# Kernel tuning notes

Measured on AMD Instinct MI355X. Metric: run time of the kernel, lower is better.

## Reference

```python
import jax, jax.numpy as jnp
import numpy as np

B, L, D, H, NL, EXP = 8, 1024, 512, 8, 6, 4
DH = D // H
DF = D * EXP
EPS = 1e-3  # keras LayerNormalization default epsilon
NEG = -1e9  # keras Softmax mask adder for float32


def _ln(x, g, b):
    m = jnp.mean(x, axis=-1, keepdims=True)
    v = jnp.mean(jnp.square(x - m), axis=-1, keepdims=True)
    return (x - m) * jax.lax.rsqrt(v + EPS) * g + b


def _pos_emb(L, D):
    pos = jnp.arange(L, dtype=jnp.float32)[:, None]          # [L,1]
    i = jnp.arange(D // 2, dtype=jnp.float32)[None, :]        # [1,D/2]
    inv = jnp.power(10000.0, -2.0 * i / D)
    # original concatenates sin block then cos block along feature axis
    return jnp.concatenate([jnp.sin(pos * inv), jnp.cos(pos * inv)], axis=-1)  # [L,D]


def setup_inputs() -> dict:
    key = jax.random.key(0)
    ks = jax.random.split(key, 16)
    glorot = lambda k, shape: jax.random.uniform(
        k, shape, jnp.float32, -1.0, 1.0) * jnp.sqrt(6.0 / (shape[-2] + shape[-1]))
    return {
        "x": jax.random.normal(ks[0], (B, L, D), jnp.float32),
        "lengths": jax.random.randint(ks[1], (B,), L // 2, L + 1).astype(jnp.int32),
        "Wq": glorot(ks[2], (NL, D, D)),
        "Wk": glorot(ks[3], (NL, D, D)),
        "Wv": glorot(ks[4], (NL, D, D)),
        "Wo": glorot(ks[5], (NL, D, D)),
        "ln1_g": jnp.ones((NL, D), jnp.float32),
        "ln1_b": jnp.zeros((NL, D), jnp.float32),
        "ln2_g": jnp.ones((NL, D), jnp.float32),
        "ln2_b": jnp.zeros((NL, D), jnp.float32),
        "w1": glorot(ks[6], (NL, D, DF)),
        "b1": jnp.zeros((NL, DF), jnp.float32),
        "w2": glorot(ks[7], (NL, DF, D)),
        "b2": jnp.zeros((NL, D), jnp.float32),
    }


def _forward(x, mask_bias, Wq, Wk, Wv, Wo, ln1_g, ln1_b, ln2_g, ln2_b, w1, b1, w2, b2):
    x = x + _pos_emb(L, D)[None, :, :]
    scale = 1.0 / jnp.sqrt(jnp.float32(DH))

    def layer(x, p):
        wq, wk, wv, wo, g1, be1, g2, be2, fw1, fb1, fw2, fb2 = p
        h = _ln(x, g1, be1)
        split = lambda t: t.reshape(B, L, H, DH).transpose(0, 2, 1, 3)  # [B,H,L,DH]
        q, k, v = split(h @ wq), split(h @ wk), split(h @ wv)
        scores = jnp.einsum("bhqd,bhkd->bhqk", q, k) * scale + mask_bias
        attn = jax.nn.softmax(scores, axis=-1)
        o = jnp.einsum("bhqk,bhkd->bhqd", attn, v)
        o = o.transpose(0, 2, 1, 3).reshape(B, L, D) @ wo
        x = x + o  # dropout is identity at inference
        h2 = _ln(x, g2, be2)
        ffn = jax.nn.relu(h2 @ fw1 + fb1) @ fw2 + fb2
        return x + ffn, None

    x, _ = jax.lax.scan(layer, x, (Wq, Wk, Wv, Wo, ln1_g, ln1_b, ln2_g, ln2_b, w1, b1, w2, b2))
    return x


def reference(x, lengths, Wq, Wk, Wv, Wo, ln1_g, ln1_b, ln2_g, ln2_b, w1, b1, w2, b2):
    mask = (jnp.arange(L)[None, :] < lengths[:, None]).astype(jnp.float32)  # [B,L]
    mask_bias = (1.0 - mask)[:, None, None, :] * NEG                        # [B,1,1,L]
    return _forward(x, mask_bias, Wq, Wk, Wv, Wo, ln1_g, ln1_b, ln2_g, ln2_b, w1, b1, w2, b2)
```

## Files before the change

kernel.cpp:

```cpp
#include <hip/hip_runtime.h>
#include <cstdint>
#include <cstddef>

#define Bz 8
#define Lz 1024
#define Dz 512
#define Hz 8
#define NLz 6
#define DFz 2048
#define Mz (Bz*Lz)

typedef short bf16x8 __attribute__((ext_vector_type(8)));
typedef float f32x4  __attribute__((ext_vector_type(4)));
typedef short s16x4  __attribute__((ext_vector_type(4)));

__device__ __forceinline__ short f2bf(float f) {
    unsigned u = __builtin_bit_cast(unsigned, f);
    u = (u + 0x7fff + ((u >> 16) & 1)) >> 16;
    return (short)u;
}

__device__ __forceinline__ float exp2_fast(float x) {
#if __has_builtin(__builtin_amdgcn_exp2f)
    return __builtin_amdgcn_exp2f(x);
#else
    return exp2f(x);
#endif
}

#define GLD16(gp, lp) __builtin_amdgcn_global_load_lds( \
    (const __attribute__((address_space(1))) void*)(gp), \
    (__attribute__((address_space(3))) void*)(lp), 16, 0, 0)

__global__ __launch_bounds__(256) void posadd_kernel(const float* __restrict__ x,
                                                     float* __restrict__ y) {
    int idx = blockIdx.x * 256 + threadIdx.x;
    int d   = idx & (Dz - 1);
    int pos = (idx >> 9) & (Lz - 1);
    int i2  = (d < Dz/2) ? d : d - Dz/2;
    float inv = __expf(-0.03597789207f * (float)i2);
    float a = (float)pos * inv;
    float pe = (d < Dz/2) ? sinf(a) : cosf(a);
    y[idx] = x[idx] + pe;
}

__global__ __launch_bounds__(256) void ln_kernel(const float* __restrict__ x,
                                                 const float* __restrict__ g,
                                                 const float* __restrict__ b,
                                                 short* __restrict__ out) {
    int w = threadIdx.x >> 6, l = threadIdx.x & 63;
    int row = blockIdx.x * 4 + w;
    const float* xr = x + (size_t)row * Dz;
    f32x4 a0 = *(const f32x4*)(xr + l * 4);
    f32x4 a1 = *(const f32x4*)(xr + 256 + l * 4);
    float s = (a0[0] + a0[1]) + (a0[2] + a0[3]) + (a1[0] + a1[1]) + (a1[2] + a1[3]);
    #pragma unroll
    for (int off = 32; off; off >>= 1) s += __shfl_xor(s, off, 64);
    float m = s * (1.0f / Dz);
    f32x4 d0, d1;
    float s2 = 0.0f;
    #pragma unroll
    for (int j = 0; j < 4; j++) { d0[j] = a0[j] - m; s2 += d0[j] * d0[j]; }
    #pragma unroll
    for (int j = 0; j < 4; j++) { d1[j] = a1[j] - m; s2 += d1[j] * d1[j]; }
    #pragma unroll
    for (int off = 32; off; off >>= 1) s2 += __shfl_xor(s2, off, 64);
    float rs = rsqrtf(s2 * (1.0f / Dz) + 1e-3f);
    f32x4 g0 = *(const f32x4*)(g + l * 4);
    f32x4 g1 = *(const f32x4*)(g + 256 + l * 4);
    f32x4 b0 = *(const f32x4*)(b + l * 4);
    f32x4 b1 = *(const f32x4*)(b + 256 + l * 4);
    s16x4 o0, o1;
    #pragma unroll
    for (int j = 0; j < 4; j++) o0[j] = f2bf(d0[j] * rs * g0[j] + b0[j]);
    #pragma unroll
    for (int j = 0; j < 4; j++) o1[j] = f2bf(d1[j] * rs * g1[j] + b1[j]);
    *(s16x4*)(out + (size_t)row * Dz + l * 4)       = o0;
    *(s16x4*)(out + (size_t)row * Dz + 256 + l * 4) = o1;
}

__global__ __launch_bounds__(256) void transpose_bf16_kernel(const float* __restrict__ src,
                                                             short* __restrict__ dst,
                                                             int K, int N,
                                                             long srcLS, long dstLS, int rowOff) {
    __shared__ float tile[32][33];
    int tx = threadIdx.x & 31, ty = threadIdx.x >> 5;
    int bx = blockIdx.x, by = blockIdx.y, z = blockIdx.z;
    const float* s = src + (size_t)z * srcLS;
    short* d = dst + (size_t)z * dstLS;
    #pragma unroll
    for (int i = 0; i < 4; i++)
        tile[ty + i * 8][tx] = s[(size_t)(by * 32 + ty + i * 8) * N + bx * 32 + tx];
    __syncthreads();
    #pragma unroll
    for (int i = 0; i < 4; i++)
        d[(size_t)(rowOff + bx * 32 + ty + i * 8) * K + by * 32 + tx] = f2bf(tile[tx][ty + i * 8]);
}

__global__ __launch_bounds__(256) void vtrans_kernel(const short* __restrict__ qkv,
                                                     short* __restrict__ vbt) {
    int lt = blockIdx.x, bh = blockIdx.y;
    int b = bh >> 3, h = bh & 7;
    __shared__ short tile[64][72];
    int t = threadIdx.x;
    int l = t >> 2, c4 = t & 3;
    #pragma unroll
    for (int p = 0; p < 2; p++) {
        int dd = (c4 + p * 4) * 8;
        *(uint4*)&tile[l][dd] =
            *(const uint4*)(qkv + ((size_t)(b * Lz + lt * 64 + l)) * 1536 + 1024 + h * 64 + dd);
    }
    __syncthreads();
    int d = t >> 2;
    #pragma unroll
    for (int p = 0; p < 2; p++) {
        int lc = (c4 + p * 4) * 8;
        union { uint4 u; short s[8]; } o;
        #pragma unroll
        for (int j = 0; j < 8; j++) o.s[j] = tile[lc + j][d];
        *(uint4*)(vbt + ((size_t)(bh * 64 + d)) * Lz + lt * 64 + lc) = o.u;
    }
}

template<int MODE, int TN>
__global__ __launch_bounds__(256, 2)
void gemm_bt(const short* __restrict__ A,
             const short* __restrict__ Bt,
             short* __restrict__ outb,
             float* __restrict__ outf,
             float* __restrict__ outf2,
             const float* __restrict__ bias,
             int M, int N, int K) {
    constexpr int NI = TN / 32;
    __shared__ __attribute__((aligned(16))) short As[128 * 64];
    __shared__ __attribute__((aligned(16))) short Bs[TN * 64];
    int t = threadIdx.x;
    int m0 = blockIdx.x * 128, n0 = blockIdx.y * TN;
    int w = t >> 6, l = t & 63;
    int wm = (w >> 1) * 64, wn = (w & 1) * (TN / 2);
    int lr = l & 15, lq = l >> 4;
    f32x4 acc[4][NI] = {};
    int sr = t >> 3;
    int sc = ((t & 7) ^ (sr & 7)) * 8;
    for (int kk = 0; kk < K; kk += 64) {
        #pragma unroll
        for (int i = 0; i < 4; i++)
            GLD16(A + (size_t)(m0 + sr + i * 32) * K + kk + sc, As + i * 2048 + t * 8);
        #pragma unroll
        for (int i = 0; i < TN / 32; i++)
            GLD16(Bt + (size_t)(n0 + sr + i * 32) * K + kk + sc, Bs + i * 2048 + t * 8);
        __syncthreads();
        bf16x8 af[4][2], bfr[NI][2];
        #pragma unroll
        for (int i = 0; i < 4; i++) {
            int row = wm + i * 16 + lr;
            const short* rp = As + row * 64;
            af[i][0] = *(const bf16x8*)(rp + ((lq ^ (row & 7)) * 8));
            af[i][1] = *(const bf16x8*)(rp + (((4 + lq) ^ (row & 7)) * 8));
        }
        #pragma unroll
        for (int i = 0; i < NI; i++) {
            int row = wn + i * 16 + lr;
            const short* rp = Bs + row * 64;
            bfr[i][0] = *(const bf16x8*)(rp + ((lq ^ (row & 7)) * 8));
            bfr[i][1] = *(const bf16x8*)(rp + (((4 + lq) ^ (row & 7)) * 8));
        }
        #pragma unroll
        for (int mi = 0; mi < 4; mi++)
            #pragma unroll
            for (int ni = 0; ni < NI; ni++) {
                acc[mi][ni] = __builtin_amdgcn_mfma_f32_16x16x32_bf16(af[mi][0], bfr[ni][0], acc[mi][ni], 0, 0, 0);
                acc[mi][ni] = __builtin_amdgcn_mfma_f32_16x16x32_bf16(af[mi][1], bfr[ni][1], acc[mi][ni], 0, 0, 0);
            }
        __syncthreads();
    }
    #pragma unroll
    for (int mi = 0; mi < 4; mi++)
        #pragma unroll
        for (int ni = 0; ni < NI; ni++) {
            int col = n0 + wn + ni * 16 + lr;
            float bv = (MODE == 2 || MODE == 3 || MODE == 4) ? bias[col] : 0.0f;
            #pragma unroll
            for (int r = 0; r < 4; r++) {
                int row = m0 + wm + mi * 16 + lq * 4 + r;
                size_t idx = (size_t)row * N + col;
                float v = acc[mi][ni][r];
                if (MODE == 0)      outb[idx] = f2bf(v);
                else if (MODE == 1) outf[idx] += v;
                else if (MODE == 2) outb[idx] = f2bf(fmaxf(v + bv, 0.0f));
                else if (MODE == 3) outf[idx] += v + bv;
                else                outf2[idx] = outf[idx] + v + bv;
            }
        }
}

__device__ __forceinline__ void attn_frag(f32x4* sacc, const float* biask,
                                          float* mr, float* lsum, f32x4* oacc,
                                          short* Pw, const short* Vs,
                                          int lr, int lq, bf16x8 onesf) {
    const float SC2 = 0.18033688f;
    float p[8][4];
    #pragma unroll
    for (int r = 0; r < 4; r++) {
        float mx = -1e30f;
        #pragma unroll
        for (int kt = 0; kt < 8; kt++) {
            p[kt][r] = sacc[kt][r] * SC2 + biask[kt];
            mx = fmaxf(mx, p[kt][r]);
        }
        mx = fmaxf(mx, __shfl_xor(mx, 1, 64));
        mx = fmaxf(mx, __shfl_xor(mx, 2, 64));
        mx = fmaxf(mx, __shfl_xor(mx, 4, 64));
        mx = fmaxf(mx, __shfl_xor(mx, 8, 64));
        float mn = fmaxf(mr[r], mx);
        float alpha = exp2_fast(mr[r] - mn);
        mr[r] = mn;
        #pragma unroll
        for (int kt = 0; kt < 8; kt++)
            p[kt][r] = exp2_fast(p[kt][r] - mn);
        lsum[r] *= alpha;
        #pragma unroll
        for (int ni = 0; ni < 4; ni++) oacc[ni][r] *= alpha;
    }
    #pragma unroll
    for (int kt = 0; kt < 8; kt++)
        #pragma unroll
        for (int r = 0; r < 4; r++)
            Pw[(lq * 4 + r) * 136 + kt * 16 + lr] = f2bf(p[kt][r]);
    f32x4 sums = {};
    #pragma unroll
    for (int c = 0; c < 4; c++) {
        bf16x8 pf = *(const bf16x8*)(Pw + lr * 136 + c * 32 + lq * 8);
        sums = __builtin_amdgcn_mfma_f32_16x16x32_bf16(pf, onesf, sums, 0, 0, 0);
        #pragma unroll
        for (int ni = 0; ni < 4; ni++) {
            bf16x8 vf = *(const bf16x8*)(Vs + (ni * 16 + lr) * 136 + c * 32 + lq * 8);
            oacc[ni] = __builtin_amdgcn_mfma_f32_16x16x32_bf16(pf, vf, oacc[ni], 0, 0, 0);
        }
    }
    #pragma unroll
    for (int r = 0; r < 4; r++) lsum[r] += sums[r];
}

__global__ __launch_bounds__(256, 2) void attn_kernel(const short* __restrict__ qkv,
                                                      const short* __restrict__ vbt,
                                                      const int* __restrict__ lengths,
                                                      short* __restrict__ o) {
    __shared__ __attribute__((aligned(16))) short Ks[128 * 72];
    __shared__ __attribute__((aligned(16))) short Vs[64 * 136];
    __shared__ __attribute__((aligned(16))) short Ps[4][16 * 136];
    int qt = blockIdx.y;
    int bh = blockIdx.x;
    int b = bh >> 3, h = bh & 7;
    int len = lengths[b];
    int t = threadIdx.x, w = t >> 6, l = t & 63;
    int lr = l & 15, lq = l >> 4;

    const short* q0 = qkv + (size_t)(b * Lz + qt * 128 + w * 32 + lr) * 1536 + h * 64 + lq * 8;
    bf16x8 qf0a = *(const bf16x8*)(q0);
    bf16x8 qf0b = *(const bf16x8*)(q0 + 32);
    bf16x8 qf1a = *(const bf16x8*)(q0 + 16 * 1536);
    bf16x8 qf1b = *(const bf16x8*)(q0 + 16 * 1536 + 32);

    int kkey = t >> 3, kd8 = (t & 7) * 8;
    int vd = t >> 4, vk8 = (t & 15) * 8;
    const short* kbaseg = qkv + (size_t)(b * Lz) * 1536 + 512 + h * 64;
    const short* vbaseg = vbt + (size_t)(bh * 64) * Lz;

    float mr0[4] = {-1e30f, -1e30f, -1e30f, -1e30f}, ls0[4] = {0.f, 0.f, 0.f, 0.f};
    float mr1[4] = {-1e30f, -1e30f, -1e30f, -1e30f}, ls1[4] = {0.f, 0.f, 0.f, 0.f};
    f32x4 oacc0[4] = {}, oacc1[4] = {};
    bf16x8 onesf = {0x3F80, 0x3F80, 0x3F80, 0x3F80, 0x3F80, 0x3F80, 0x3F80, 0x3F80};

    uint4 kreg[4], vreg[4];
    #pragma unroll
    for (int i = 0; i < 4; i++)
        kreg[i] = *(const uint4*)(kbaseg + (size_t)(i * 32 + kkey) * 1536 + kd8);

    short* Pw = &Ps[w][0];
    int ntiles = (len + 127) >> 7;
    for (int tix = 0; tix < ntiles; tix++) {
        int k0 = tix << 7;
        __syncthreads();
        #pragma unroll
        for (int i = 0; i < 4; i++)
            *(uint4*)(Ks + (i * 32 + kkey) * 72 + kd8) = kreg[i];
        __syncthreads();
        #pragma unroll
        for (int i = 0; i < 4; i++)
            vreg[i] = *(const uint4*)(vbaseg + (size_t)(i * 16 + vd) * Lz + k0 + vk8);
        f32x4 sacc0[8] = {}, sacc1[8] = {};
        #pragma unroll
        for (int kt = 0; kt < 8; kt++) {
            bf16x8 kf0 = *(const bf16x8*)(Ks + (kt * 16 + lr) * 72 + lq * 8);
            bf16x8 kf1 = *(const bf16x8*)(Ks + (kt * 16 + lr) * 72 + 32 + lq * 8);
            sacc0[kt] = __builtin_amdgcn_mfma_f32_16x16x32_bf16(qf0a, kf0, sacc0[kt], 0, 0, 0);
            sacc0[kt] = __builtin_amdgcn_mfma_f32_16x16x32_bf16(qf0b, kf1, sacc0[kt], 0, 0, 0);
            sacc1[kt] = __builtin_amdgcn_mfma_f32_16x16x32_bf16(qf1a, kf0, sacc1[kt], 0, 0, 0);
            sacc1[kt] = __builtin_amdgcn_mfma_f32_16x16x32_bf16(qf1b, kf1, sacc1[kt], 0, 0, 0);
        }
        if (tix + 1 < ntiles) {
            #pragma unroll
            for (int i = 0; i < 4; i++)
                kreg[i] = *(const uint4*)(kbaseg + (size_t)(k0 + 128 + i * 32 + kkey) * 1536 + kd8);
        }
        #pragma unroll
        for (int i = 0; i < 4; i++)
            *(uint4*)(Vs + (i * 16 + vd) * 136 + vk8) = vreg[i];
        float biask[8];
        #pragma unroll
        for (int kt = 0; kt < 8; kt++)
            biask[kt] = ((k0 + kt * 16 + lr) < len) ? 0.0f : -1e30f;
        __syncthreads();
        attn_frag(sacc0, biask, mr0, ls0, oacc0, Pw, Vs, lr, lq, onesf);
        attn_frag(sacc1, biask, mr1, ls1, oacc1, Pw, Vs, lr, lq, onesf);
    }
    #pragma unroll
    for (int ni = 0; ni < 4; ni++)
        #pragma unroll
        for (int r = 0; r < 4; r++) {
            int q = qt * 128 + w * 32 + lq * 4 + r;
            size_t base = (size_t)(b * Lz + q) * Dz + h * 64 + ni * 16 + lr;
            o[base]             = f2bf(oacc0[ni][r] / ls0[r]);
            o[base + 16 * Dz]   = f2bf(oacc1[ni][r] / ls1[r]);
        }
}

extern "C" void kernel_launch(void* const* d_in, const int* in_sizes, int n_in,
                              void* d_out, int out_size, void* d_ws, size_t ws_size,
                              hipStream_t stream) {
    const float* x_in    = (const float*)d_in[0];
    const int*   lengths = (const int*)d_in[1];
    const float* Wq   = (const float*)d_in[2];
    const float* Wk   = (const float*)d_in[3];
    const float* Wv   = (const float*)d_in[4];
    const float* Wo   = (const float*)d_in[5];
    const float* ln1g = (const float*)d_in[6];
    const float* ln1b = (const float*)d_in[7];
    const float* ln2g = (const float*)d_in[8];
    const float* ln2b = (const float*)d_in[9];
    const float* w1   = (const float*)d_in[10];
    const float* b1   = (const float*)d_in[11];
    const float* w2   = (const float*)d_in[12];
    const float* b2   = (const float*)d_in[13];

    size_t off = 0;
    auto alloc = [&](size_t bytes) {
        void* p = (char*)d_ws + off;
        off += (bytes + 255) & ~(size_t)255;
        return p;
    };
    float* x_work = (float*)alloc((size_t)Mz * Dz * 4);
    short* hbuf   = (short*)alloc((size_t)Mz * Dz * 2);
    short* qkvb   = (short*)alloc((size_t)Mz * 1536 * 2);
    short* f1b    = (short*)alloc((size_t)Mz * DFz * 2);
    short* vbt    = (short*)alloc((size_t)Bz * Hz * 64 * Lz * 2);
    short* wqkvT  = (short*)alloc((size_t)NLz * 1536 * Dz * 2);
    short* woT    = (short*)alloc((size_t)NLz * Dz * Dz * 2);
    short* w1T    = (short*)alloc((size_t)NLz * DFz * Dz * 2);
    short* w2T    = (short*)alloc((size_t)NLz * Dz * DFz * 2);

    dim3 tb(256);
    transpose_bf16_kernel<<<dim3(16, 16, NLz), tb, 0, stream>>>(Wq, wqkvT, Dz, Dz, (long)Dz*Dz, (long)1536*Dz, 0);
    transpose_bf16_kernel<<<dim3(16, 16, NLz), tb, 0, stream>>>(Wk, wqkvT, Dz, Dz, (long)Dz*Dz, (long)1536*Dz, 512);
    transpose_bf16_kernel<<<dim3(16, 16, NLz), tb, 0, stream>>>(Wv, wqkvT, Dz, Dz, (long)Dz*Dz, (long)1536*Dz, 1024);
    transpose_bf16_kernel<<<dim3(16, 16, NLz), tb, 0, stream>>>(Wo, woT, Dz, Dz, (long)Dz*Dz, (long)Dz*Dz, 0);
    transpose_bf16_kernel<<<dim3(64, 16, NLz), tb, 0, stream>>>(w1, w1T, Dz, DFz, (long)Dz*DFz, (long)DFz*Dz, 0);
    transpose_bf16_kernel<<<dim3(16, 64, NLz), tb, 0, stream>>>(w2, w2T, DFz, Dz, (long)DFz*Dz, (long)Dz*DFz, 0);

    posadd_kernel<<<dim3(Mz * Dz / 256), tb, 0, stream>>>(x_in, x_work);

    for (int lyr = 0; lyr < NLz; lyr++) {
        const short* wqkvL = wqkvT + (size_t)lyr * 1536 * Dz;
        const short* woL   = woT   + (size_t)lyr * Dz * Dz;
        const short* w1L   = w1T   + (size_t)lyr * DFz * Dz;
        const short* w2L   = w2T   + (size_t)lyr * Dz * DFz;

        ln_kernel<<<dim3(Mz/4), tb, 0, stream>>>(x_work, ln1g + lyr * Dz, ln1b + lyr * Dz, hbuf);
        gemm_bt<0,128><<<dim3(Mz/128, 1536/128), tb, 0, stream>>>(hbuf, wqkvL, qkvb, nullptr, nullptr, nullptr, Mz, 1536, Dz);
        vtrans_kernel<<<dim3(Lz/64, Bz*Hz), tb, 0, stream>>>(qkvb, vbt);
        attn_kernel<<<dim3(Bz*Hz, Lz/128), tb, 0, stream>>>(qkvb, vbt, lengths, hbuf);
        gemm_bt<1,64><<<dim3(Mz/128, Dz/64), tb, 0, stream>>>(hbuf, woL, nullptr, x_work, nullptr, nullptr, Mz, Dz, Dz);
        ln_kernel<<<dim3(Mz/4), tb, 0, stream>>>(x_work, ln2g + lyr * Dz, ln2b + lyr * Dz, hbuf);
        gemm_bt<2,128><<<dim3(Mz/128, DFz/128), tb, 0, stream>>>(hbuf, w1L, f1b, nullptr, nullptr, b1 + lyr * DFz, Mz, DFz, Dz);
        if (lyr < NLz - 1)
            gemm_bt<3,64><<<dim3(Mz/128, Dz/64), tb, 0, stream>>>(f1b, w2L, nullptr, x_work, nullptr, b2 + lyr * Dz, Mz, Dz, DFz);
        else
            gemm_bt<4,64><<<dim3(Mz/128, Dz/64), tb, 0, stream>>>(f1b, w2L, nullptr, x_work, (float*)d_out, b2 + lyr * Dz, Mz, Dz, DFz);
    }
}
```

Baseline: 1.056 ms.

## Double-buffer FFN2 GEMM LDS tiles and lazily rescale attention softmax

Adds a double-buffered variant of the bf16 GEMM. It issues the next K-tile's global-to-LDS loads before computing on the current tile, with one barrier per iteration. Only the long-K FFN-down GEMM uses it, and it doubles that kernel's LDS footprint. The attention online softmax now skips the running-max update and the rescaling of accumulators and sums unless the new max exceeds the old one by more than 8 (log2 units) anywhere in the wavefront. This cuts exp and multiply work at the cost of allowing unnormalised probabilities up to 256.

```diff
diff --git a/kernel.cpp b/kernel.cpp
--- a/kernel.cpp
+++ b/kernel.cpp
@@ -122,7 +122,36 @@
     }
 }
 
-template<int MODE, int TN>
+template<int NI>
+__device__ __forceinline__ void gemm_step(const short* __restrict__ Ab,
+                                          const short* __restrict__ Bb,
+                                          f32x4 (*acc)[NI],
+                                          int wm, int wn, int lr, int lq) {
+    bf16x8 af[4][2], bfr[NI][2];
+    #pragma unroll
+    for (int i = 0; i < 4; i++) {
+        int row = wm + i * 16 + lr;
+        const short* rp = Ab + row * 64;
+        af[i][0] = *(const bf16x8*)(rp + ((lq ^ (row & 7)) * 8));
+        af[i][1] = *(const bf16x8*)(rp + (((4 + lq) ^ (row & 7)) * 8));
+    }
+    #pragma unroll
+    for (int i = 0; i < NI; i++) {
+        int row = wn + i * 16 + lr;
+        const short* rp = Bb + row * 64;
+        bfr[i][0] = *(const bf16x8*)(rp + ((lq ^ (row & 7)) * 8));
+        bfr[i][1] = *(const bf16x8*)(rp + (((4 + lq) ^ (row & 7)) * 8));
+    }
+    #pragma unroll
+    for (int mi = 0; mi < 4; mi++)
+        #pragma unroll
+        for (int ni = 0; ni < NI; ni++) {
+            acc[mi][ni] = __builtin_amdgcn_mfma_f32_16x16x32_bf16(af[mi][0], bfr[ni][0], acc[mi][ni], 0, 0, 0);
+            acc[mi][ni] = __builtin_amdgcn_mfma_f32_16x16x32_bf16(af[mi][1], bfr[ni][1], acc[mi][ni], 0, 0, 0);
+        }
+}
+
+template<int MODE, int TN, int DBUF>
 __global__ __launch_bounds__(256, 2)
 void gemm_bt(const short* __restrict__ A,
              const short* __restrict__ Bt,
@@ -132,8 +161,10 @@
              const float* __restrict__ bias,
              int M, int N, int K) {
     constexpr int NI = TN / 32;
-    __shared__ __attribute__((aligned(16))) short As[128 * 64];
-    __shared__ __attribute__((aligned(16))) short Bs[TN * 64];
+    constexpr int ASZ = 128 * 64;
+    constexpr int BSZ = TN * 64;
+    __shared__ __attribute__((aligned(16))) short As[(DBUF ? 2 : 1) * ASZ];
+    __shared__ __attribute__((aligned(16))) short Bs[(DBUF ? 2 : 1) * BSZ];
     int t = threadIdx.x;
     int m0 = blockIdx.x * 128, n0 = blockIdx.y * TN;
     int w = t >> 6, l = t & 63;
@@ -142,38 +173,46 @@
     f32x4 acc[4][NI] = {};
     int sr = t >> 3;
     int sc = ((t & 7) ^ (sr & 7)) * 8;
-    for (int kk = 0; kk < K; kk += 64) {
+
+    if constexpr (!DBUF) {
+        for (int kk = 0; kk < K; kk += 64) {
+            #pragma unroll
+            for (int i = 0; i < 4; i++)
+                GLD16(A + (size_t)(m0 + sr + i * 32) * K + kk + sc, As + i * 2048 + t * 8);
+            #pragma unroll
+            for (int i = 0; i < TN / 32; i++)
+                GLD16(Bt + (size_t)(n0 + sr + i * 32) * K + kk + sc, Bs + i * 2048 + t * 8);
+            __syncthreads();
+            gemm_step<NI>(As, Bs, acc, wm, wn, lr, lq);
+            __syncthreads();
+        }
+    } else {
+        int nt = K >> 6;
         #pragma unroll
         for (int i = 0; i < 4; i++)
-            GLD16(A + (size_t)(m0 + sr + i * 32) * K + kk + sc, As + i * 2048 + t * 8);
+            GLD16(A + (size_t)(m0 + sr + i * 32) * K + sc, As + i * 2048 + t * 8);
         #pragma unroll
         for (int i = 0; i < TN / 32; i++)
-            GLD16(Bt + (size_t)(n0 + sr + i * 32) * K + kk + sc, Bs + i * 2048 + t * 8);
+            GLD16(Bt + (size_t)(n0 + sr + i * 32) * K + sc, Bs + i * 2048 + t * 8);
         __syncthreads();
-        bf16x8 af[4][2], bfr[NI][2];
-        #pragma unroll
-        for (int i = 0; i < 4; i++) {
-            int row = wm + i * 16 + lr;
-            const short* rp = As + row * 64;
-            af[i][0] = *(const bf16x8*)(rp + ((lq ^ (row & 7)) * 8));
-            af[i][1] = *(const bf16x8*)(rp + (((4 + lq) ^ (row & 7)) * 8));
-        }
-        #pragma unroll
-        for (int i = 0; i < NI; i++) {
-            int row = wn + i * 16 + lr;
-            const short* rp = Bs + row * 64;
-            bfr[i][0] = *(const bf16x8*)(rp + ((lq ^ (row & 7)) * 8));
-            bfr[i][1] = *(const bf16x8*)(rp + (((4 + lq) ^ (row & 7)) * 8));
-        }
-        #pragma unroll
-        for (int mi = 0; mi < 4; mi++)
-            #pragma unroll
-            for (int ni = 0; ni < NI; ni++) {
-                acc[mi][ni] = __builtin_amdgcn_mfma_f32_16x16x32_bf16(af[mi][0], bfr[ni][0], acc[mi][ni], 0, 0, 0);
-                acc[mi][ni] = __builtin_amdgcn_mfma_f32_16x16x32_bf16(af[mi][1], bfr[ni][1], acc[mi][ni], 0, 0, 0);
+        for (int tix = 0; tix < nt; ++tix) {
+            int cur = tix & 1;
+            if (tix + 1 < nt) {
+                short* Ad = As + (cur ^ 1) * ASZ;
+                short* Bd = Bs + (cur ^ 1) * BSZ;
+                int kk = (tix + 1) << 6;
+                #pragma unroll
+                for (int i = 0; i < 4; i++)
+                    GLD16(A + (size_t)(m0 + sr + i * 32) * K + kk + sc, Ad + i * 2048 + t * 8);
+                #pragma unroll
+                for (int i = 0; i < TN / 32; i++)
+                    GLD16(Bt + (size_t)(n0 + sr + i * 32) * K + kk + sc, Bd + i * 2048 + t * 8);
             }
-        __syncthreads();
-    }
+            gemm_step<NI>(As + cur * ASZ, Bs + cur * BSZ, acc, wm, wn, lr, lq);
+            __syncthreads();
+        }
+    }
+
     #pragma unroll
     for (int mi = 0; mi < 4; mi++)
         #pragma unroll
@@ -212,15 +251,17 @@
         mx = fmaxf(mx, __shfl_xor(mx, 2, 64));
         mx = fmaxf(mx, __shfl_xor(mx, 4, 64));
         mx = fmaxf(mx, __shfl_xor(mx, 8, 64));
-        float mn = fmaxf(mr[r], mx);
-        float alpha = exp2_fast(mr[r] - mn);
-        mr[r] = mn;
+        if (!__all(mx <= mr[r] + 8.0f)) {
+            float mn = fmaxf(mr[r], mx);
+            float alpha = exp2_fast(mr[r] - mn);
+            mr[r] = mn;
+            lsum[r] *= alpha;
+            #pragma unroll
+            for (int ni = 0; ni < 4; ni++) oacc[ni][r] *= alpha;
+        }
         #pragma unroll
         for (int kt = 0; kt < 8; kt++)
-            p[kt][r] = exp2_fast(p[kt][r] - mn);
-        lsum[r] *= alpha;
-        #pragma unroll
-        for (int ni = 0; ni < 4; ni++) oacc[ni][r] *= alpha;
+            p[kt][r] = exp2_fast(p[kt][r] - mr[r]);
     }
     #pragma unroll
     for (int kt = 0; kt < 8; kt++)
@@ -377,15 +418,15 @@
         const short* w2L   = w2T   + (size_t)lyr * Dz * DFz;
 
         ln_kernel<<<dim3(Mz/4), tb, 0, stream>>>(x_work, ln1g + lyr * Dz, ln1b + lyr * Dz, hbuf);
-        gemm_bt<0,128><<<dim3(Mz/128, 1536/128), tb, 0, stream>>>(hbuf, wqkvL, qkvb, nullptr, nullptr, nullptr, Mz, 1536, Dz);
+        gemm_bt<0,128,0><<<dim3(Mz/128, 1536/128), tb, 0, stream>>>(hbuf, wqkvL, qkvb, nullptr, nullptr, nullptr, Mz, 1536, Dz);
         vtrans_kernel<<<dim3(Lz/64, Bz*Hz), tb, 0, stream>>>(qkvb, vbt);
         attn_kernel<<<dim3(Bz*Hz, Lz/128), tb, 0, stream>>>(qkvb, vbt, lengths, hbuf);
-        gemm_bt<1,64><<<dim3(Mz/128, Dz/64), tb, 0, stream>>>(hbuf, woL, nullptr, x_work, nullptr, nullptr, Mz, Dz, Dz);
+        gemm_bt<1,64,0><<<dim3(Mz/128, Dz/64), tb, 0, stream>>>(hbuf, woL, nullptr, x_work, nullptr, nullptr, Mz, Dz, Dz);
         ln_kernel<<<dim3(Mz/4), tb, 0, stream>>>(x_work, ln2g + lyr * Dz, ln2b + lyr * Dz, hbuf);
-        gemm_bt<2,128><<<dim3(Mz/128, DFz/128), tb, 0, stream>>>(hbuf, w1L, f1b, nullptr, nullptr, b1 + lyr * DFz, Mz, DFz, Dz);
+        gemm_bt<2,128,0><<<dim3(Mz/128, DFz/128), tb, 0, stream>>>(hbuf, w1L, f1b, nullptr, nullptr, b1 + lyr * DFz, Mz, DFz, Dz);
         if (lyr < NLz - 1)
-            gemm_bt<3,64><<<dim3(Mz/128, Dz/64), tb, 0, stream>>>(f1b, w2L, nullptr, x_work, nullptr, b2 + lyr * Dz, Mz, Dz, DFz);
+            gemm_bt<3,64,1><<<dim3(Mz/128, Dz/64), tb, 0, stream>>>(f1b, w2L, nullptr, x_work, nullptr, b2 + lyr * Dz, Mz, Dz, DFz);
         else
-            gemm_bt<4,64><<<dim3(Mz/128, Dz/64), tb, 0, stream>>>(f1b, w2L, nullptr, x_work, (float*)d_out, b2 + lyr * Dz, Mz, Dz, DFz);
-    }
-}
+            gemm_bt<4,64,1><<<dim3(Mz/128, Dz/64), tb, 0, stream>>>(f1b, w2L, nullptr, x_work, (float*)d_out, b2 + lyr * Dz, Mz, Dz, DFz);
+    }
+}
```

Result: no change. 1.074 ms (+1.7%).
